# Optimization experiments

Hardware: AMD Instinct MI355X
Metric: run time of the kernel (lower is better)

## Reference

```python
import jax, jax.numpy as jnp
import numpy as np

N, U, V = 512, 2048, 43          # batch, phoneme seq len, vocab (Phoneme43)
H, K, NCLASS = 512, 10, 512      # hidden, GMM components, 2**bit
EPS = 1e-5


def gru_cell(x, h, wih, whh, bih, bhh):
    # PyTorch GRU gate order: r, z, n
    gi = x @ wih.T + bih          # [N, 3H]
    gh = h @ whh.T + bhh          # [N, 3H]
    gi_r, gi_z, gi_n = jnp.split(gi, 3, axis=1)
    gh_r, gh_z, gh_n = jnp.split(gh, 3, axis=1)
    r = jax.nn.sigmoid(gi_r + gh_r)
    z = jax.nn.sigmoid(gi_z + gh_z)
    n = jnp.tanh(gi_n + r * gh_n)
    return (1.0 - z) * n + z * h


def setup_inputs() -> dict:
    key = jax.random.key(0)
    ks = jax.random.split(key, 20)
    s = 0.05  # keep exp() arguments tame
    inp = {
        "xt": jax.random.normal(ks[0], (N,), jnp.float32),
        "cx": jax.random.uniform(ks[1], (N, U, V), jnp.float32),
        "encoder_hidden": jax.random.normal(ks[2], (1, N, H), jnp.float32),
        "wt_1": jax.random.normal(ks[3], (N, V), jnp.float32) * s,
        "h2t_1": jax.random.normal(ks[4], (1, N, H), jnp.float32),
        "h3t_1": jax.random.uniform(ks[5], (1, N, H), jnp.float32),
        "kappa_t_1": jax.random.uniform(ks[6], (N, K), jnp.float32),
        # learned params
        "Wh1p_w": jax.random.normal(ks[7], (3 * K, H + V), jnp.float32) * s,
        "Wh1p_b": jax.random.normal(ks[8], (3 * K,), jnp.float32) * s,
        "rnn2_wih": jax.random.normal(ks[9], (3 * H, 1 + V), jnp.float32) * s,
        "rnn2_whh": jax.random.normal(ks[10], (3 * H, H), jnp.float32) * s,
        "rnn2_bih": jax.random.normal(ks[11], (3 * H,), jnp.float32) * s,
        "rnn2_bhh": jax.random.normal(ks[12], (3 * H,), jnp.float32) * s,
        "rnn3_wih": jax.random.normal(ks[13], (3 * H, H), jnp.float32) * s,
        "rnn3_whh": jax.random.normal(ks[14], (3 * H, H), jnp.float32) * s,
        "rnn3_bih": jax.random.normal(ks[15], (3 * H,), jnp.float32) * s,
        "rnn3_bhh": jax.random.normal(ks[16], (3 * H,), jnp.float32) * s,
        "Y_w": jax.random.normal(ks[17], (NCLASS, H), jnp.float32) * s,
        "Y_b": jax.random.normal(ks[18], (NCLASS,), jnp.float32) * s,
    }
    return inp


def reference(xt, cx, encoder_hidden, wt_1, h2t_1, h3t_1, kappa_t_1,
              Wh1p_w, Wh1p_b, rnn2_wih, rnn2_whh, rnn2_bih, rnn2_bhh,
              rnn3_wih, rnn3_whh, rnn3_bih, rnn3_bhh, Y_w, Y_b):
    eh = encoder_hidden[0]                                   # [N, H]
    abk = jnp.concatenate([eh, wt_1], axis=1) @ Wh1p_w.T + Wh1p_b  # [N, 3K]
    alpha = jnp.exp(abk[:, :K]) + EPS                        # [N, K]
    beta = jnp.exp(abk[:, K:2 * K]) + EPS                    # [N, K]
    kappa = kappa_t_1 + jnp.exp(abk[:, 2 * K:3 * K])         # [N, K]
    u = jnp.arange(cx.shape[1], dtype=cx.dtype)              # [U]
    # Graves GMM attention window: phi[n,u] = sum_k alpha * exp(-beta*(kappa-u)^2)
    phi = jnp.sum(alpha[:, :, None] *
                  jnp.exp(-beta[:, :, None] * (kappa[:, :, None] - u) ** 2),
                  axis=1)                                    # [N, U]
    wt = jnp.einsum("nuv,nu->nv", cx, phi)                  # [N, V]
    x2 = jnp.concatenate([xt[:, None], wt], axis=1)          # [N, 1+V]
    h2 = gru_cell(x2, h2t_1[0], rnn2_wih, rnn2_whh, rnn2_bih, rnn2_bhh)
    res = h2
    h3 = gru_cell(jax.nn.relu(h2), h3t_1[0], rnn3_wih, rnn3_whh, rnn3_bih, rnn3_bhh)
    out = h3 + res                                           # [N, H]
    dist = jax.nn.relu(out) @ Y_w.T + Y_b                    # [N, n_class]
    dist = dist[:, None, :]                                  # [N, 1, n_class] (transpose(0,1) of [1,N,C])
    return dist, h2[None], h3[None], phi, wt, kappa
```

## Files before the change

kernel.cpp:

```cpp
#include <hip/hip_runtime.h>
#include <math.h>

typedef unsigned short ushortT;
typedef __attribute__((ext_vector_type(8))) short bf16x8;
typedef __attribute__((ext_vector_type(8))) unsigned short u16x8;
typedef __attribute__((ext_vector_type(4))) float f32x4;
typedef float f32x4u __attribute__((ext_vector_type(4), aligned(4)));

#define NN   512
#define UU   2048
#define VV   43
#define HH   512
#define KMIX 10
#define NCLS 512
#define EPSF 1e-5f
#define KCAT 555

#define OFF_DIST  0
#define OFF_H2    262144
#define OFF_H3    524288
#define OFF_PHI   786432
#define OFF_WT    1835008
#define OFF_KAPPA 1857024

__device__ __forceinline__ ushortT f2bf(float f) {
    unsigned int u = __builtin_bit_cast(unsigned int, f);
    u = (u + 0x7fffu + ((u >> 16) & 1u)) >> 16;
    return (ushortT)u;
}

__device__ __forceinline__ u16x8 cv8(float4 lo, float4 hi) {
    u16x8 o;
    o[0]=f2bf(lo.x); o[1]=f2bf(lo.y); o[2]=f2bf(lo.z); o[3]=f2bf(lo.w);
    o[4]=f2bf(hi.x); o[5]=f2bf(hi.y); o[6]=f2bf(hi.z); o[7]=f2bf(hi.w);
    return o;
}

__global__ __launch_bounds__(256, 2) void attn_kernel(
    const float* __restrict__ xt, const float* __restrict__ cx,
    const float* __restrict__ eh, const float* __restrict__ wt_1,
    const float* __restrict__ Ww, const float* __restrict__ Wb,
    const float* __restrict__ kappa_prev,
    float* __restrict__ phi_out, float* __restrict__ wt_out,
    float* __restrict__ kappa_out, ushortT* __restrict__ A2)
{
    __shared__ float x[KCAT];
    __shared__ float sm[32];
    __shared__ float aL[KMIX], bL[KMIX], kL[KMIX], um[KMIX];
    __shared__ float red[4*VV];
    __shared__ float wtv[VV+1];

    int n = blockIdx.x, t = threadIdx.x;
    int lane = t & 63, wid = t >> 6;
    const float* cxn = cx + (size_t)n*UU*VV;

    const float* rowp0 = cxn + (size_t)t*VV;
    f32x4u r0[10]; f32x4u rt0;
#pragma unroll
    for (int q = 0; q < 10; ++q) r0[q] = *(const f32x4u*)(rowp0 + q*4);
    rt0 = *(const f32x4u*)(rowp0 + 39);

    for (int i = t; i < KCAT; i += 256)
        x[i] = (i < HH) ? eh[(size_t)n*HH + i] : wt_1[n*VV + (i - HH)];
    __syncthreads();
#pragma unroll
    for (int rr = 0; rr < 8; ++rr) {
        int g = rr*4 + wid;
        float v = 0.f;
        if (g < 30) {
            const float* w = Ww + (size_t)g*KCAT;
#pragma unroll
            for (int q = 0; q < 9; ++q) {
                int i = q*64 + lane;
                if (i < KCAT) v += x[i]*w[i];
            }
        }
        v += __shfl_xor(v, 32, 64); v += __shfl_xor(v, 16, 64); v += __shfl_xor(v, 8, 64);
        v += __shfl_xor(v, 4, 64);  v += __shfl_xor(v, 2, 64);  v += __shfl_xor(v, 1, 64);
        if (lane == 0 && g < 30) sm[g] = v;
    }
    __syncthreads();
    if (t < 30) {
        float ev = __expf(sm[t] + Wb[t]);
        if (t < 10)       aL[t] = ev + EPSF;
        else if (t < 20)  bL[t-10] = ev + EPSF;
        else { float kap = kappa_prev[n*KMIX + (t-20)] + ev; kL[t-20] = kap;
               kappa_out[n*KMIX + (t-20)] = kap; }
    }
    __syncthreads();
    if (t < KMIX)
        um[t] = kL[t] + sqrtf(fmaxf(60.f + __logf(aL[t]), 0.f) / bL[t]);
    __syncthreads();
    float ulim = um[0];
#pragma unroll
    for (int k = 1; k < KMIX; ++k) ulim = fmaxf(ulim, um[k]);
    int nchunks = min(8, (int)(ulim) / 256 + 1);
    nchunks = __builtin_amdgcn_readfirstlane(nchunks);

    float phi_reg[8];
#pragma unroll
    for (int c = 0; c < 8; ++c) {
        int u = c*256 + t; float uu = (float)u, s = 0.f;
#pragma unroll
        for (int k = 0; k < KMIX; ++k) { float d = kL[k] - uu; s += aL[k]*__expf(-bL[k]*d*d); }
        phi_reg[c] = s;
        phi_out[(size_t)n*UU + u] = s;
    }

    float acc[VV];
    {
        float p = phi_reg[0];
#pragma unroll
        for (int q = 0; q < 10; ++q) {
            acc[q*4+0] = r0[q].x*p; acc[q*4+1] = r0[q].y*p;
            acc[q*4+2] = r0[q].z*p; acc[q*4+3] = r0[q].w*p;
        }
        acc[40] = rt0.y*p; acc[41] = rt0.z*p; acc[42] = rt0.w*p;
    }
#pragma unroll
    for (int c = 1; c < 8; ++c) {
        if (c < nchunks) {
            const float* rowp = cxn + (size_t)(c*256 + t)*VV;
            f32x4u r[10];
#pragma unroll
            for (int q = 0; q < 10; ++q) r[q] = *(const f32x4u*)(rowp + q*4);
            f32x4u rt = *(const f32x4u*)(rowp + 39);
            float p = phi_reg[c];
#pragma unroll
            for (int q = 0; q < 10; ++q) {
                acc[q*4+0] += r[q].x*p; acc[q*4+1] += r[q].y*p;
                acc[q*4+2] += r[q].z*p; acc[q*4+3] += r[q].w*p;
            }
            acc[40] += rt.y*p; acc[41] += rt.z*p; acc[42] += rt.w*p;
        }
    }

#pragma unroll
    for (int v = 0; v < VV; ++v) {
        float val = acc[v];
#pragma unroll
        for (int off = 32; off > 0; off >>= 1) val += __shfl_down(val, off, 64);
        if (lane == 0) red[wid*VV + v] = val;
    }
    __syncthreads();
    if (t < VV) {
        float w4 = red[t] + red[VV+t] + red[2*VV+t] + red[3*VV+t];
        wt_out[n*VV + t] = w4; wtv[t] = w4;
    }
    __syncthreads();
    if (t < 64) {
        float v = (t == 0) ? xt[n] : (t < 44 ? wtv[t-1] : 0.f);
        A2[(size_t)n*64 + t] = f2bf(v);
    }
}

template<int NG, int NSA, int NSB, int EPI, int WIK>
__global__ __launch_bounds__(256) void gemm_fused(
    const ushortT* __restrict__ Ai, const float* __restrict__ Wi,
    const float* __restrict__ Ah, const float* __restrict__ Wh,
    const float* __restrict__ bih, const float* __restrict__ bhh,
    const float* __restrict__ hprev, const float* __restrict__ resv,
    float* __restrict__ outF, ushortT* __restrict__ outB, const float* __restrict__ Yb)
{
    constexpr int NS = NSA + NSB;
    __shared__ ushortT lds0[(NG+1)*32*64];
    __shared__ ushortT lds1[(NG+1)*32*64];

    int tid = threadIdx.x, lane = tid & 63, wid = tid >> 6;
    int wm = wid >> 1, wj = wid & 1;
    int bj0 = blockIdx.x*32, bm0 = blockIdx.y*32;
    int fcol = lane & 15, g2 = lane >> 4;
    int arow = tid >> 3, aslot = tid & 7;

    float4 stgA[NG+1][2], stgB[NG+1][2];
    const float4 fz = {0.f, 0.f, 0.f, 0.f};

    auto loadregs = [&](int s, float4 (&dst)[NG+1][2]) {
        if (s < NSA) {
            dst[0][0] = *(const float4*)(Ai + (size_t)(bm0 + arow)*(NSA*64) + s*64 + aslot*8);
#pragma unroll
            for (int q = 1; q <= NG; ++q) {
                int unit = (q-1)*256 + tid;
                int brow = unit >> 3, bslot = unit & 7;
                int gate = brow >> 5, r = brow & 31;
                int col = s*64 + bslot*8;
                const float* src = Wi + (size_t)(gate*512 + bj0 + r)*WIK + col;
                if constexpr (WIK % 64 != 0) {
                    dst[q][0] = (col + 4 <= WIK) ? *(const float4*)src : fz;
                    dst[q][1] = (col + 8 <= WIK) ? *(const float4*)(src + 4) : fz;
                } else {
                    dst[q][0] = *(const float4*)src;
                    dst[q][1] = *(const float4*)(src + 4);
                }
            }
        } else {
            int kb = (s - NSA)*64;
            const float* srcA = Ah + (size_t)(bm0 + arow)*512 + kb + aslot*8;
            dst[0][0] = *(const float4*)srcA;
            dst[0][1] = *(const float4*)(srcA + 4);
#pragma unroll
            for (int q = 1; q <= NG; ++q) {
                int unit = (q-1)*256 + tid;
                int brow = unit >> 3, bslot = unit & 7;
                int gate = brow >> 5, r = brow & 31;
                const float* src = Wh + (size_t)(gate*512 + bj0 + r)*512 + kb + bslot*8;
                dst[q][0] = *(const float4*)src;
                dst[q][1] = *(const float4*)(src + 4);
            }
        }
    };
    auto stow = [&](int s, const float4 (&src)[NG+1][2], ushortT* buf) {
        if (s < NSA) {
            *(float4*)(buf + arow*64 + (aslot ^ (arow & 7))*8) = src[0][0];
        } else {
            *(u16x8*)(buf + arow*64 + (aslot ^ (arow & 7))*8) = cv8(src[0][0], src[0][1]);
        }
#pragma unroll
        for (int q = 1; q <= NG; ++q) {
            int unit = (q-1)*256 + tid;
            int brow = unit >> 3, bslot = unit & 7;
            *(u16x8*)(buf + 2048 + brow*64 + (bslot ^ (brow & 7))*8) = cv8(src[q][0], src[q][1]);
        }
    };

    f32x4 aR = {0.f,0.f,0.f,0.f}, aZ = {0.f,0.f,0.f,0.f};
    f32x4 aN1 = {0.f,0.f,0.f,0.f}, aN2 = {0.f,0.f,0.f,0.f};

    int ra = wm*16 + fcol, rb = wj*16 + fcol;

    loadregs(0, stgA);
    stow(0, stgA, lds0);
    if (NS > 1) loadregs(1, stgB);
    __syncthreads();

#pragma unroll
    for (int s = 0; s < NS; ++s) {
        ushortT* cur = (s & 1) ? lds1 : lds0;
        ushortT* nxt = (s & 1) ? lds0 : lds1;
        if (s + 2 < NS) {
            if (s & 1) loadregs(s + 2, stgB); else loadregs(s + 2, stgA);
        }
        bf16x8 af0 = *(const bf16x8*)(cur + ra*64 + ((g2    ) ^ (ra & 7))*8);
        bf16x8 af1 = *(const bf16x8*)(cur + ra*64 + ((4 + g2) ^ (ra & 7))*8);
        bf16x8 b0[NG], b1[NG];
#pragma unroll
        for (int g = 0; g < NG; ++g) {
            int rbt = g*32 + rb;
            b0[g] = *(const bf16x8*)(cur + 2048 + rbt*64 + ((g2    ) ^ (rbt & 7))*8);
            b1[g] = *(const bf16x8*)(cur + 2048 + rbt*64 + ((4 + g2) ^ (rbt & 7))*8);
        }
        if (s + 1 < NS) {
            if (s & 1) stow(s + 1, stgA, nxt); else stow(s + 1, stgB, nxt);
        }
        aR = __builtin_amdgcn_mfma_f32_16x16x32_bf16(af0, b0[0], aR, 0, 0, 0);
        aR = __builtin_amdgcn_mfma_f32_16x16x32_bf16(af1, b1[0], aR, 0, 0, 0);
        if constexpr (NG >= 2) {
            aZ = __builtin_amdgcn_mfma_f32_16x16x32_bf16(af0, b0[1], aZ, 0, 0, 0);
            aZ = __builtin_amdgcn_mfma_f32_16x16x32_bf16(af1, b1[1], aZ, 0, 0, 0);
        }
        if constexpr (NG >= 3) {
            if (s < NSA) {
                aN1 = __builtin_amdgcn_mfma_f32_16x16x32_bf16(af0, b0[2], aN1, 0, 0, 0);
                aN1 = __builtin_amdgcn_mfma_f32_16x16x32_bf16(af1, b1[2], aN1, 0, 0, 0);
            } else {
                aN2 = __builtin_amdgcn_mfma_f32_16x16x32_bf16(af0, b0[2], aN2, 0, 0, 0);
                aN2 = __builtin_amdgcn_mfma_f32_16x16x32_bf16(af1, b1[2], aN2, 0, 0, 0);
            }
        }
        __syncthreads();
    }

    int row0 = bm0 + wm*16 + (lane >> 4)*4;
    int col  = bj0 + wj*16 + fcol;
    if constexpr (EPI == 0) {
        float b = Yb[col];
#pragma unroll
        for (int e = 0; e < 4; ++e)
            outF[(size_t)(row0 + e)*512 + col] = aR[e] + b;
    } else {
        float b_r  = bih[col] + bhh[col];
        float b_z  = bih[512 + col] + bhh[512 + col];
        float b_ni = bih[1024 + col];
        float b_nh = bhh[1024 + col];
#pragma unroll
        for (int e = 0; e < 4; ++e) {
            size_t off = (size_t)(row0 + e)*512 + col;
            float r  = 1.f/(1.f + __expf(-(aR[e] + b_r)));
            float z  = 1.f/(1.f + __expf(-(aZ[e] + b_z)));
            float nn = tanhf(aN1[e] + b_ni + r*(aN2[e] + b_nh));
            float h  = (1.f - z)*nn + z*hprev[off];
            outF[off] = h;
            float xo = (EPI == 2) ? (h + resv[off]) : h;
            outB[off] = f2bf(fmaxf(xo, 0.f));
        }
    }
}

extern "C" void kernel_launch(void* const* d_in, const int* in_sizes, int n_in,
                              void* d_out, int out_size, void* d_ws, size_t ws_size,
                              hipStream_t stream)
{
    const float* xt   = (const float*)d_in[0];
    const float* cx   = (const float*)d_in[1];
    const float* eh   = (const float*)d_in[2];
    const float* wt_1 = (const float*)d_in[3];
    const float* h2p  = (const float*)d_in[4];
    const float* h3p  = (const float*)d_in[5];
    const float* kp   = (const float*)d_in[6];
    const float* Ww   = (const float*)d_in[7];
    const float* Wb   = (const float*)d_in[8];
    const float* w2ih = (const float*)d_in[9];
    const float* w2hh = (const float*)d_in[10];
    const float* b2ih = (const float*)d_in[11];
    const float* b2hh = (const float*)d_in[12];
    const float* w3ih = (const float*)d_in[13];
    const float* w3hh = (const float*)d_in[14];
    const float* b3ih = (const float*)d_in[15];
    const float* b3hh = (const float*)d_in[16];
    const float* Yw   = (const float*)d_in[17];
    const float* Yb   = (const float*)d_in[18];

    float* out = (float*)d_out;
    float* dist = out + OFF_DIST;
    float* h2o  = out + OFF_H2;
    float* h3o  = out + OFF_H3;
    float* phi  = out + OFF_PHI;
    float* wto  = out + OFF_WT;
    float* kapo = out + OFF_KAPPA;

    char* p = (char*)d_ws;
    ushortT* A2  = (ushortT*)p;  p += (size_t)512*64*2;
    ushortT* A3i = (ushortT*)p;  p += (size_t)512*512*2;
    ushortT* Ad  = (ushortT*)p;  p += (size_t)512*512*2;

    attn_kernel<<<NN, 256, 0, stream>>>(xt, cx, eh, wt_1, Ww, Wb, kp, phi, wto, kapo, A2);
    gemm_fused<3, 1, 8, 1, 44><<<dim3(16, 16), 256, 0, stream>>>(
        A2, w2ih, h2p, w2hh, b2ih, b2hh, h2p, nullptr, h2o, A3i, nullptr);
    gemm_fused<3, 8, 8, 2, 512><<<dim3(16, 16), 256, 0, stream>>>(
        A3i, w3ih, h3p, w3hh, b3ih, b3hh, h3p, h2o, h3o, Ad, nullptr);
    gemm_fused<1, 8, 0, 0, 512><<<dim3(16, 16), 256, 0, stream>>>(
        Ad, Yw, h2p, w2hh, nullptr, nullptr, nullptr, nullptr, dist, nullptr, Yb);
}
```

Measured before the change: 61.47 us.

## Hoist hidden-state GRU GEMMs into the attention kernel launch

The recurrent h@Whh products for both GRU layers depend only on inputs, so they now run as extra blocks inside the attention kernel launch (1024 blocks: 512 attention and 512 GEMM tiles). Their pre-activations go to workspace planes, and the later GRU kernels only do the input GEMM and read those planes in the epilogue. This shortens the serial dependency chain and overlaps the GEMM work with the memory-bound attention pass. The cost is extra global writes and reads of six 512x512 float planes, plus a shared-memory union that may lower attention-block occupancy.

```diff
diff --git a/kernel.cpp b/kernel.cpp
--- a/kernel.cpp
+++ b/kernel.cpp
@@ -15,6 +15,7 @@
 #define NCLS 512
 #define EPSF 1e-5f
 #define KCAT 555
+#define PLANE 262144
 
 #define OFF_DIST  0
 #define OFF_H2    262144
@@ -36,139 +37,27 @@
     return o;
 }
 
-__global__ __launch_bounds__(256, 2) void attn_kernel(
-    const float* __restrict__ xt, const float* __restrict__ cx,
-    const float* __restrict__ eh, const float* __restrict__ wt_1,
-    const float* __restrict__ Ww, const float* __restrict__ Wb,
-    const float* __restrict__ kappa_prev,
-    float* __restrict__ phi_out, float* __restrict__ wt_out,
-    float* __restrict__ kappa_out, ushortT* __restrict__ A2)
-{
-    __shared__ float x[KCAT];
-    __shared__ float sm[32];
-    __shared__ float aL[KMIX], bL[KMIX], kL[KMIX], um[KMIX];
-    __shared__ float red[4*VV];
-    __shared__ float wtv[VV+1];
-
-    int n = blockIdx.x, t = threadIdx.x;
-    int lane = t & 63, wid = t >> 6;
-    const float* cxn = cx + (size_t)n*UU*VV;
-
-    const float* rowp0 = cxn + (size_t)t*VV;
-    f32x4u r0[10]; f32x4u rt0;
-#pragma unroll
-    for (int q = 0; q < 10; ++q) r0[q] = *(const f32x4u*)(rowp0 + q*4);
-    rt0 = *(const f32x4u*)(rowp0 + 39);
-
-    for (int i = t; i < KCAT; i += 256)
-        x[i] = (i < HH) ? eh[(size_t)n*HH + i] : wt_1[n*VV + (i - HH)];
-    __syncthreads();
-#pragma unroll
-    for (int rr = 0; rr < 8; ++rr) {
-        int g = rr*4 + wid;
-        float v = 0.f;
-        if (g < 30) {
-            const float* w = Ww + (size_t)g*KCAT;
-#pragma unroll
-            for (int q = 0; q < 9; ++q) {
-                int i = q*64 + lane;
-                if (i < KCAT) v += x[i]*w[i];
-            }
-        }
-        v += __shfl_xor(v, 32, 64); v += __shfl_xor(v, 16, 64); v += __shfl_xor(v, 8, 64);
-        v += __shfl_xor(v, 4, 64);  v += __shfl_xor(v, 2, 64);  v += __shfl_xor(v, 1, 64);
-        if (lane == 0 && g < 30) sm[g] = v;
-    }
-    __syncthreads();
-    if (t < 30) {
-        float ev = __expf(sm[t] + Wb[t]);
-        if (t < 10)       aL[t] = ev + EPSF;
-        else if (t < 20)  bL[t-10] = ev + EPSF;
-        else { float kap = kappa_prev[n*KMIX + (t-20)] + ev; kL[t-20] = kap;
-               kappa_out[n*KMIX + (t-20)] = kap; }
-    }
-    __syncthreads();
-    if (t < KMIX)
-        um[t] = kL[t] + sqrtf(fmaxf(60.f + __logf(aL[t]), 0.f) / bL[t]);
-    __syncthreads();
-    float ulim = um[0];
-#pragma unroll
-    for (int k = 1; k < KMIX; ++k) ulim = fmaxf(ulim, um[k]);
-    int nchunks = min(8, (int)(ulim) / 256 + 1);
-    nchunks = __builtin_amdgcn_readfirstlane(nchunks);
-
-    float phi_reg[8];
-#pragma unroll
-    for (int c = 0; c < 8; ++c) {
-        int u = c*256 + t; float uu = (float)u, s = 0.f;
-#pragma unroll
-        for (int k = 0; k < KMIX; ++k) { float d = kL[k] - uu; s += aL[k]*__expf(-bL[k]*d*d); }
-        phi_reg[c] = s;
-        phi_out[(size_t)n*UU + u] = s;
-    }
-
-    float acc[VV];
-    {
-        float p = phi_reg[0];
-#pragma unroll
-        for (int q = 0; q < 10; ++q) {
-            acc[q*4+0] = r0[q].x*p; acc[q*4+1] = r0[q].y*p;
-            acc[q*4+2] = r0[q].z*p; acc[q*4+3] = r0[q].w*p;
-        }
-        acc[40] = rt0.y*p; acc[41] = rt0.z*p; acc[42] = rt0.w*p;
-    }
-#pragma unroll
-    for (int c = 1; c < 8; ++c) {
-        if (c < nchunks) {
-            const float* rowp = cxn + (size_t)(c*256 + t)*VV;
-            f32x4u r[10];
-#pragma unroll
-            for (int q = 0; q < 10; ++q) r[q] = *(const f32x4u*)(rowp + q*4);
-            f32x4u rt = *(const f32x4u*)(rowp + 39);
-            float p = phi_reg[c];
-#pragma unroll
-            for (int q = 0; q < 10; ++q) {
-                acc[q*4+0] += r[q].x*p; acc[q*4+1] += r[q].y*p;
-                acc[q*4+2] += r[q].z*p; acc[q*4+3] += r[q].w*p;
-            }
-            acc[40] += rt.y*p; acc[41] += rt.z*p; acc[42] += rt.w*p;
-        }
-    }
-
-#pragma unroll
-    for (int v = 0; v < VV; ++v) {
-        float val = acc[v];
-#pragma unroll
-        for (int off = 32; off > 0; off >>= 1) val += __shfl_down(val, off, 64);
-        if (lane == 0) red[wid*VV + v] = val;
-    }
-    __syncthreads();
-    if (t < VV) {
-        float w4 = red[t] + red[VV+t] + red[2*VV+t] + red[3*VV+t];
-        wt_out[n*VV + t] = w4; wtv[t] = w4;
-    }
-    __syncthreads();
-    if (t < 64) {
-        float v = (t == 0) ? xt[n] : (t < 44 ? wtv[t-1] : 0.f);
-        A2[(size_t)n*64 + t] = f2bf(v);
-    }
-}
-
-template<int NG, int NSA, int NSB, int EPI, int WIK>
-__global__ __launch_bounds__(256) void gemm_fused(
+struct AttnS {
+    float x[KCAT];
+    float sm[32];
+    float aL[KMIX], bL[KMIX], kL[KMIX], um[KMIX];
+    float red[4*VV];
+    float wtv[VV+1];
+};
+
+template<int NG, int NSA, int NSB, int EPI, int WIK, int MODE>
+__device__ __forceinline__ void gemm_body(
+    int bj0, int bm0, ushortT* lds0, ushortT* lds1,
     const ushortT* __restrict__ Ai, const float* __restrict__ Wi,
     const float* __restrict__ Ah, const float* __restrict__ Wh,
     const float* __restrict__ bih, const float* __restrict__ bhh,
     const float* __restrict__ hprev, const float* __restrict__ resv,
-    float* __restrict__ outF, ushortT* __restrict__ outB, const float* __restrict__ Yb)
+    float* __restrict__ outF, ushortT* __restrict__ outB,
+    const float* __restrict__ Yb, float* __restrict__ preC)
 {
     constexpr int NS = NSA + NSB;
-    __shared__ ushortT lds0[(NG+1)*32*64];
-    __shared__ ushortT lds1[(NG+1)*32*64];
-
     int tid = threadIdx.x, lane = tid & 63, wid = tid >> 6;
     int wm = wid >> 1, wj = wid & 1;
-    int bj0 = blockIdx.x*32, bm0 = blockIdx.y*32;
     int fcol = lane & 15, g2 = lane >> 4;
     int arow = tid >> 3, aslot = tid & 7;
 
@@ -272,7 +161,16 @@
 
     int row0 = bm0 + wm*16 + (lane >> 4)*4;
     int col  = bj0 + wj*16 + fcol;
-    if constexpr (EPI == 0) {
+
+    if constexpr (MODE == 1) {
+#pragma unroll
+        for (int e = 0; e < 4; ++e) {
+            size_t off = (size_t)(row0 + e)*512 + col;
+            preC[off]           = aR[e];
+            preC[PLANE + off]   = aZ[e];
+            preC[2*PLANE + off] = aN2[e];
+        }
+    } else if constexpr (EPI == 0) {
         float b = Yb[col];
 #pragma unroll
         for (int e = 0; e < 4; ++e)
@@ -285,15 +183,175 @@
 #pragma unroll
         for (int e = 0; e < 4; ++e) {
             size_t off = (size_t)(row0 + e)*512 + col;
-            float r  = 1.f/(1.f + __expf(-(aR[e] + b_r)));
-            float z  = 1.f/(1.f + __expf(-(aZ[e] + b_z)));
-            float nn = tanhf(aN1[e] + b_ni + r*(aN2[e] + b_nh));
+            float gr = aR[e], gz = aZ[e], gnh = aN2[e];
+            if constexpr (MODE == 2) {
+                gr  += preC[off];
+                gz  += preC[PLANE + off];
+                gnh  = preC[2*PLANE + off];
+            }
+            float r  = 1.f/(1.f + __expf(-(gr + b_r)));
+            float z  = 1.f/(1.f + __expf(-(gz + b_z)));
+            float nn = tanhf(aN1[e] + b_ni + r*(gnh + b_nh));
             float h  = (1.f - z)*nn + z*hprev[off];
             outF[off] = h;
             float xo = (EPI == 2) ? (h + resv[off]) : h;
             outB[off] = f2bf(fmaxf(xo, 0.f));
         }
     }
+}
+
+__global__ __launch_bounds__(256) void attn_gh(
+    const float* __restrict__ xt, const float* __restrict__ cx,
+    const float* __restrict__ eh, const float* __restrict__ wt_1,
+    const float* __restrict__ Ww, const float* __restrict__ Wb,
+    const float* __restrict__ kappa_prev,
+    float* __restrict__ phi_out, float* __restrict__ wt_out,
+    float* __restrict__ kappa_out, ushortT* __restrict__ A2,
+    const float* __restrict__ h2p, const float* __restrict__ w2hh,
+    const float* __restrict__ h3p, const float* __restrict__ w3hh,
+    float* __restrict__ gh2C, float* __restrict__ gh3C)
+{
+    __shared__ __align__(16) ushortT smem[2][4*32*64];
+    int bb = blockIdx.x, t = threadIdx.x;
+
+    if (bb >= NN) {
+        int gb = bb - NN;
+        int sub = gb & 255;
+        int bj0 = (sub & 15)*32, bm0 = (sub >> 4)*32;
+        if (gb < 256)
+            gemm_body<3, 0, 8, 1, 512, 1>(bj0, bm0, &smem[0][0], &smem[1][0],
+                nullptr, nullptr, h2p, w2hh, nullptr, nullptr, nullptr, nullptr,
+                nullptr, nullptr, nullptr, gh2C);
+        else
+            gemm_body<3, 0, 8, 1, 512, 1>(bj0, bm0, &smem[0][0], &smem[1][0],
+                nullptr, nullptr, h3p, w3hh, nullptr, nullptr, nullptr, nullptr,
+                nullptr, nullptr, nullptr, gh3C);
+        return;
+    }
+
+    AttnS* S = (AttnS*)&smem[0][0];
+    int n = bb;
+    int lane = t & 63, wid = t >> 6;
+    const float* cxn = cx + (size_t)n*UU*VV;
+
+    const float* rowp0 = cxn + (size_t)t*VV;
+    f32x4u r0[10]; f32x4u rt0;
+#pragma unroll
+    for (int q = 0; q < 10; ++q) r0[q] = *(const f32x4u*)(rowp0 + q*4);
+    rt0 = *(const f32x4u*)(rowp0 + 39);
+
+    for (int i = t; i < KCAT; i += 256)
+        S->x[i] = (i < HH) ? eh[(size_t)n*HH + i] : wt_1[n*VV + (i - HH)];
+    __syncthreads();
+#pragma unroll
+    for (int rr = 0; rr < 8; ++rr) {
+        int g = rr*4 + wid;
+        float v = 0.f;
+        if (g < 30) {
+            const float* w = Ww + (size_t)g*KCAT;
+#pragma unroll
+            for (int q = 0; q < 9; ++q) {
+                int i = q*64 + lane;
+                if (i < KCAT) v += S->x[i]*w[i];
+            }
+        }
+        v += __shfl_xor(v, 32, 64); v += __shfl_xor(v, 16, 64); v += __shfl_xor(v, 8, 64);
+        v += __shfl_xor(v, 4, 64);  v += __shfl_xor(v, 2, 64);  v += __shfl_xor(v, 1, 64);
+        if (lane == 0 && g < 30) S->sm[g] = v;
+    }
+    __syncthreads();
+    if (t < 30) {
+        float ev = __expf(S->sm[t] + Wb[t]);
+        if (t < 10)       S->aL[t] = ev + EPSF;
+        else if (t < 20)  S->bL[t-10] = ev + EPSF;
+        else { float kap = kappa_prev[n*KMIX + (t-20)] + ev; S->kL[t-20] = kap;
+               kappa_out[n*KMIX + (t-20)] = kap; }
+    }
+    __syncthreads();
+    if (t < KMIX)
+        S->um[t] = S->kL[t] + sqrtf(fmaxf(60.f + __logf(S->aL[t]), 0.f) / S->bL[t]);
+    __syncthreads();
+    float ulim = S->um[0];
+#pragma unroll
+    for (int k = 1; k < KMIX; ++k) ulim = fmaxf(ulim, S->um[k]);
+    int nchunks = min(8, (int)(ulim) / 256 + 1);
+    nchunks = __builtin_amdgcn_readfirstlane(nchunks);
+
+    float aL[KMIX], bL[KMIX], kL[KMIX];
+#pragma unroll
+    for (int k = 0; k < KMIX; ++k) { aL[k] = S->aL[k]; bL[k] = S->bL[k]; kL[k] = S->kL[k]; }
+
+    float phi_reg[8];
+#pragma unroll
+    for (int c = 0; c < 8; ++c) {
+        int u = c*256 + t; float uu = (float)u, s = 0.f;
+#pragma unroll
+        for (int k = 0; k < KMIX; ++k) { float d = kL[k] - uu; s += aL[k]*__expf(-bL[k]*d*d); }
+        phi_reg[c] = s;
+        phi_out[(size_t)n*UU + u] = s;
+    }
+
+    float acc[VV];
+    {
+        float p = phi_reg[0];
+#pragma unroll
+        for (int q = 0; q < 10; ++q) {
+            acc[q*4+0] = r0[q].x*p; acc[q*4+1] = r0[q].y*p;
+            acc[q*4+2] = r0[q].z*p; acc[q*4+3] = r0[q].w*p;
+        }
+        acc[40] = rt0.y*p; acc[41] = rt0.z*p; acc[42] = rt0.w*p;
+    }
+#pragma unroll
+    for (int c = 1; c < 8; ++c) {
+        if (c < nchunks) {
+            const float* rowp = cxn + (size_t)(c*256 + t)*VV;
+            f32x4u r[10];
+#pragma unroll
+            for (int q = 0; q < 10; ++q) r[q] = *(const f32x4u*)(rowp + q*4);
+            f32x4u rt = *(const f32x4u*)(rowp + 39);
+            float p = phi_reg[c];
+#pragma unroll
+            for (int q = 0; q < 10; ++q) {
+                acc[q*4+0] += r[q].x*p; acc[q*4+1] += r[q].y*p;
+                acc[q*4+2] += r[q].z*p; acc[q*4+3] += r[q].w*p;
+            }
+            acc[40] += rt.y*p; acc[41] += rt.z*p; acc[42] += rt.w*p;
+        }
+    }
+
+#pragma unroll
+    for (int v = 0; v < VV; ++v) {
+        float val = acc[v];
+#pragma unroll
+        for (int off = 32; off > 0; off >>= 1) val += __shfl_down(val, off, 64);
+        if (lane == 0) S->red[wid*VV + v] = val;
+    }
+    __syncthreads();
+    if (t < VV) {
+        float w4 = S->red[t] + S->red[VV+t] + S->red[2*VV+t] + S->red[3*VV+t];
+        wt_out[n*VV + t] = w4; S->wtv[t] = w4;
+    }
+    __syncthreads();
+    if (t < 64) {
+        float v = (t == 0) ? xt[n] : (t < 44 ? S->wtv[t-1] : 0.f);
+        A2[(size_t)n*64 + t] = f2bf(v);
+    }
+}
+
+template<int NG, int NSA, int NSB, int EPI, int WIK, int MODE>
+__global__ __launch_bounds__(256) void gemm_k(
+    const ushortT* __restrict__ Ai, const float* __restrict__ Wi,
+    const float* __restrict__ Ah, const float* __restrict__ Wh,
+    const float* __restrict__ bih, const float* __restrict__ bhh,
+    const float* __restrict__ hprev, const float* __restrict__ resv,
+    float* __restrict__ outF, ushortT* __restrict__ outB,
+    const float* __restrict__ Yb, float* __restrict__ preC)
+{
+    __shared__ __align__(16) ushortT lds0[(NG+1)*32*64];
+    __shared__ __align__(16) ushortT lds1[(NG+1)*32*64];
+    gemm_body<NG, NSA, NSB, EPI, WIK, MODE>(
+        blockIdx.x*32, blockIdx.y*32, lds0, lds1,
+        Ai, Wi, Ah, Wh, bih, bhh, hprev, resv, outF, outB, Yb, preC);
 }
 
 extern "C" void kernel_launch(void* const* d_in, const int* in_sizes, int n_in,
@@ -329,15 +387,19 @@
     float* kapo = out + OFF_KAPPA;
 
     char* p = (char*)d_ws;
-    ushortT* A2  = (ushortT*)p;  p += (size_t)512*64*2;
-    ushortT* A3i = (ushortT*)p;  p += (size_t)512*512*2;
-    ushortT* Ad  = (ushortT*)p;  p += (size_t)512*512*2;
-
-    attn_kernel<<<NN, 256, 0, stream>>>(xt, cx, eh, wt_1, Ww, Wb, kp, phi, wto, kapo, A2);
-    gemm_fused<3, 1, 8, 1, 44><<<dim3(16, 16), 256, 0, stream>>>(
-        A2, w2ih, h2p, w2hh, b2ih, b2hh, h2p, nullptr, h2o, A3i, nullptr);
-    gemm_fused<3, 8, 8, 2, 512><<<dim3(16, 16), 256, 0, stream>>>(
-        A3i, w3ih, h3p, w3hh, b3ih, b3hh, h3p, h2o, h3o, Ad, nullptr);
-    gemm_fused<1, 8, 0, 0, 512><<<dim3(16, 16), 256, 0, stream>>>(
-        Ad, Yw, h2p, w2hh, nullptr, nullptr, nullptr, nullptr, dist, nullptr, Yb);
-}
+    ushortT* A2   = (ushortT*)p;  p += (size_t)512*64*2;
+    ushortT* A3i  = (ushortT*)p;  p += (size_t)512*512*2;
+    ushortT* Ad   = (ushortT*)p;  p += (size_t)512*512*2;
+    float*   gh2C = (float*)p;    p += (size_t)3*PLANE*4;
+    float*   gh3C = (float*)p;    p += (size_t)3*PLANE*4;
+
+    attn_gh<<<1024, 256, 0, stream>>>(
+        xt, cx, eh, wt_1, Ww, Wb, kp, phi, wto, kapo, A2,
+        h2p, w2hh, h3p, w3hh, gh2C, gh3C);
+    gemm_k<3, 1, 0, 1, 44, 2><<<dim3(16, 16), 256, 0, stream>>>(
+        A2, w2ih, nullptr, nullptr, b2ih, b2hh, h2p, nullptr, h2o, A3i, nullptr, gh2C);
+    gemm_k<3, 8, 0, 2, 512, 2><<<dim3(16, 16), 256, 0, stream>>>(
+        A3i, w3ih, nullptr, nullptr, b3ih, b3hh, h3p, h2o, h3o, Ad, nullptr, gh3C);
+    gemm_k<1, 8, 0, 0, 512, 0><<<dim3(16, 16), 256, 0, stream>>>(
+        Ad, Yw, nullptr, nullptr, nullptr, nullptr, nullptr, nullptr, dist, nullptr, Yb, nullptr);
+}
```

New measurement: 50.75 us. -17.4%, faster.
